# Kernel tuning notes

Measured on AMD Instinct MI355X. Metric: run time of the kernel, lower is better.

The kernel has to match this reference:

```python
import jax, jax.numpy as jnp
import numpy as np
import math

L, K, B = 16, 2048, 2
BATCH = 4
N = K * B


def _pe(k, b_beats):
    # PositionalEncoding buffer: pe[features_dim=K, num_of_beats=B]
    pos = jnp.arange(k, dtype=jnp.float32)[:, None]                      # (K, 1)
    div = jnp.exp(jnp.arange(0, b_beats, 2, dtype=jnp.float32) * (-math.log(10000.0) / b_beats))
    pe = jnp.zeros((k, b_beats), dtype=jnp.float32)
    pe = pe.at[:, 0::2].set(jnp.sin(pos * div))
    pe = pe.at[:, 1::2].set(jnp.cos(pos * div))
    return pe                                                            # (K, B)


def setup_inputs() -> dict:
    key = jax.random.key(0)
    ks = jax.random.split(key, 10)
    return {
        "X": jax.random.normal(ks[0], (BATCH, L, N), jnp.float32),
        "S": jax.random.normal(ks[1], (BATCH, L, N), jnp.float32),
        "W_1x": jax.random.normal(ks[2], (L, L), jnp.float32),
        "W_1s": jax.random.normal(ks[3], (L, L), jnp.float32),
        "W_2x": jax.random.normal(ks[4], (K, K), jnp.float32),
        "W_2s": jax.random.normal(ks[5], (K, K), jnp.float32),
        "conv_wx": jax.random.normal(ks[6], (2 * L, 2 * L, 3, 3), jnp.float32) * 0.05,
        "conv_bx": jnp.zeros((2 * L,), jnp.float32),
        "conv_ws": jax.random.normal(ks[7], (2 * L, 2 * L, 3, 3), jnp.float32) * 0.05,
        "conv_bs": jnp.zeros((2 * L,), jnp.float32),
    }


def _branch(E, W2):
    # E: (b, L, N). A = softmax(E^T E, axis=2); Ea = E @ A; then K-dim mixing by W2.
    b = E.shape[0]
    A = jax.nn.softmax(jnp.einsum('bln,blm->bnm', E, E), axis=2)         # (b, N, N)
    Ea = jnp.einsum('bln,bnm->blm', E, A)                                # (b, L, N)
    Ea4 = Ea.reshape(b, L, K, B)
    M = jnp.einsum('blkt,kj->bljt', Ea4, W2)                             # (b, L, K, B)
    return M.reshape(b, L, N)


def _conv(x, w, bias):
    y = jax.lax.conv_general_dilated(x, w, (1, 1), 'SAME',
                                     dimension_numbers=('NCHW', 'OIHW', 'NCHW'))
    return y + bias[None, :, None, None]


def reference(X, S, W_1x, W_1s, W_2x, W_2s, conv_wx, conv_bx, conv_ws, conv_bs):
    b = X.shape[0]
    Xe = jnp.einsum('bln,lm->bmn', S, W_1x)
    Se = jnp.einsum('bln,lm->bmn', X, W_1s)
    Mx = _branch(Xe, W_2x)
    Ms = _branch(Se, W_2s)
    X_hat = jnp.concatenate((Mx * X, X), axis=1).reshape(b, 2 * L, K, B)
    S_hat = jnp.concatenate((Ms * S, S), axis=1).reshape(b, 2 * L, K, B)
    # positional encoding broadcast over (batch, 2L); dropout in eval mode = identity
    S_hat = S_hat + _pe(K, B)[None, None]
    X_e_hat = _conv(X_hat, conv_wx, conv_bx)
    S_e_hat = _conv(S_hat, conv_ws, conv_bs)
    return jnp.concatenate((X_e_hat, S_e_hat), axis=1)                   # (b, 4L, K, B)
```

## Files before the change

kernel.cpp:

```cpp
#include <hip/hip_runtime.h>
#include <math.h>

#define TPB 256

static constexpr int LL = 16;
static constexpr int KK = 2048;
static constexpr int NBATCH = 4;
static constexpr int NN = 4096;
static constexpr int BBR = 8;

static constexpr size_t OFF_EHL = 0;
static constexpr size_t OFF_ET  = 524288;
static constexpr size_t OFF_EAT = 819200;
static constexpr size_t OFF_PB  = 2129920;
static constexpr size_t OFF_PMX = 3178496;
static constexpr size_t OFF_PSM = 3244032;
static constexpr size_t OFF_PMM = 3309568;

typedef unsigned short ushortT;
typedef __attribute__((ext_vector_type(8))) short short8v;
typedef __attribute__((ext_vector_type(4))) float f32x4;
typedef __attribute__((ext_vector_type(16))) float f32x16;

__device__ __forceinline__ ushortT f2bf(float x) {
  union { float f; unsigned int u; } c; c.f = x;
  unsigned int u = c.u;
  return (ushortT)((u + 0x7FFFu + ((u >> 16) & 1u)) >> 16);
}
__device__ __forceinline__ float bf2f(ushortT h) {
  union { unsigned int u; float f; } c; c.u = ((unsigned int)h) << 16;
  return c.f;
}
__device__ __forceinline__ float exp2a(float x) {
  float r; asm("v_exp_f32 %0, %1" : "=v"(r) : "v"(x)); return r;
}

__global__ __launch_bounds__(TPB) void prep_kernel(
    const float* __restrict__ X, const float* __restrict__ S,
    const float* __restrict__ W1x, const float* __restrict__ W1s,
    ushortT* __restrict__ Ehl, ushortT* __restrict__ Ept) {
  __shared__ float wsh[256];
  __shared__ ushortT tl[16][272];
  const int tid = threadIdx.x;
  const int br = blockIdx.z;
  wsh[tid] = br ? W1s[tid] : W1x[tid];
  __syncthreads();
  const int n0 = blockIdx.x * 256;
  const int b = blockIdx.y;
  const int n = n0 + tid;
  const float SC = 1.2011224087f;
  const int wq = tid & 31;
  const int slot = (wq < 16) ? ((wq >> 2) * 8 + (wq & 3))
                             : (((wq - 16) >> 2) * 8 + 4 + (wq & 3));
  const int ptid = (tid & ~31) | slot;
  const float* In = br ? X : S;

  float in[16];
#pragma unroll
  for (int l = 0; l < 16; ++l)
    in[l] = In[(size_t)(b * 16 + l) * NN + n];
  float e[16];
#pragma unroll
  for (int m = 0; m < 16; ++m) {
    float a0 = 0.f;
#pragma unroll
    for (int l = 0; l < 16; ++l) a0 = fmaf(in[l], wsh[l * 16 + m], a0);
    e[m] = a0;
  }
  const int bbr = br * 4 + b;
  unsigned int rw[16];
#pragma unroll
  for (int q = 0; q < 16; ++q) rw[q] = 0;
#pragma unroll
  for (int k = 0; k < 16; ++k) {
    const float vs = e[k] * SC;
    ushortT h = f2bf(vs);
    ushortT lo = f2bf(vs - bf2f(h));
    rw[k >> 1] |= ((unsigned int)h) << (16 * (k & 1));
    rw[8 + (k >> 1)] |= ((unsigned int)lo) << (16 * (k & 1));
    tl[k][ptid] = f2bf(e[k]);
  }
  uint4* dst = (uint4*)(Ehl + ((size_t)bbr * NN + n) * 32);
  dst[0] = make_uint4(rw[0], rw[1], rw[2], rw[3]);
  dst[1] = make_uint4(rw[4], rw[5], rw[6], rw[7]);
  dst[2] = make_uint4(rw[8], rw[9], rw[10], rw[11]);
  dst[3] = make_uint4(rw[12], rw[13], rw[14], rw[15]);
  __syncthreads();
  {
    const int r = tid >> 4, c0 = (tid & 15) * 16;
    const uint4* src = (const uint4*)(&tl[r][c0]);
    uint4* d2 = (uint4*)(Ept + ((size_t)bbr * 16 + r) * NN + n0 + c0);
    d2[0] = src[0];
    d2[1] = src[1];
  }
}

__global__ __launch_bounds__(TPB) void passA_kernel(
    const ushortT* __restrict__ Ehl, float* __restrict__ pmx,
    float* __restrict__ psm) {
  const int bid = blockIdx.x;
  const int bbr = bid & 7;
  const int ms = (bid >> 3) & 1;
  const int n0 = (bid >> 4) * 64;
  const int tid = threadIdx.x;
  const int w = tid >> 6, lane = tid & 63;
  const int lc = lane & 31;
  const int koff = (lane >> 5) * 8;
  const ushortT* Eb = Ehl + (size_t)bbr * NN * 32;

  short8v bh[2], bl[2];
#pragma unroll
  for (int s = 0; s < 2; ++s) {
    const ushortT* rp = Eb + (size_t)(n0 + s * 32 + lc) * 32;
    bh[s] = *(const short8v*)(rp + koff);
    bl[s] = *(const short8v*)(rp + 16 + koff);
  }
  float mx[2] = {-INFINITY, -INFINITY};
  float sm[2] = {0.f, 0.f};
  const f32x16 z16 = {0.f, 0.f, 0.f, 0.f, 0.f, 0.f, 0.f, 0.f,
                      0.f, 0.f, 0.f, 0.f, 0.f, 0.f, 0.f, 0.f};
  const ushortT* ap = Eb + (size_t)(ms * 2048 + w * 512 + lc) * 32;
  for (int ch = 0; ch < 16; ++ch) {
    short8v ah = *(const short8v*)(ap + koff);
    short8v al = *(const short8v*)(ap + 16 + koff);
    ap += 32 * 32;
#pragma unroll
    for (int s = 0; s < 2; ++s) {
      f32x16 c = __builtin_amdgcn_mfma_f32_32x32x16_bf16(ah, bh[s], z16, 0, 0, 0);
      c = __builtin_amdgcn_mfma_f32_32x32x16_bf16(al, bh[s], c, 0, 0, 0);
      c = __builtin_amdgcn_mfma_f32_32x32x16_bf16(ah, bl[s], c, 0, 0, 0);
      float t0 = fmaxf(fmaxf(c[0], c[1]), fmaxf(c[2], c[3]));
      float t1 = fmaxf(fmaxf(c[4], c[5]), fmaxf(c[6], c[7]));
      float t2 = fmaxf(fmaxf(c[8], c[9]), fmaxf(c[10], c[11]));
      float t3 = fmaxf(fmaxf(c[12], c[13]), fmaxf(c[14], c[15]));
      float tm = fmaxf(fmaxf(t0, t1), fmaxf(t2, t3));
      if (tm > mx[s] + 30.f) {
        sm[s] *= exp2a(mx[s] - tm);
        mx[s] = tm;
      }
      float e0 = exp2a(c[0] - mx[s]) + exp2a(c[1] - mx[s]);
      float e1 = exp2a(c[2] - mx[s]) + exp2a(c[3] - mx[s]);
      float e2 = exp2a(c[4] - mx[s]) + exp2a(c[5] - mx[s]);
      float e3 = exp2a(c[6] - mx[s]) + exp2a(c[7] - mx[s]);
      float e4 = exp2a(c[8] - mx[s]) + exp2a(c[9] - mx[s]);
      float e5 = exp2a(c[10] - mx[s]) + exp2a(c[11] - mx[s]);
      float e6 = exp2a(c[12] - mx[s]) + exp2a(c[13] - mx[s]);
      float e7 = exp2a(c[14] - mx[s]) + exp2a(c[15] - mx[s]);
      sm[s] += ((e0 + e1) + (e2 + e3)) + ((e4 + e5) + (e6 + e7));
    }
  }
#pragma unroll
  for (int s = 0; s < 2; ++s) {
    float omx = __shfl_xor(mx[s], 32);
    float osm = __shfl_xor(sm[s], 32);
    float nm = fmaxf(mx[s], omx);
    sm[s] = sm[s] * exp2a(mx[s] - nm) + osm * exp2a(omx - nm);
    mx[s] = nm;
  }
  __shared__ float smx[4][2][32], ssm[4][2][32];
  if (lane < 32) {
#pragma unroll
    for (int s = 0; s < 2; ++s) {
      smx[w][s][lc] = mx[s];
      ssm[w][s][lc] = sm[s];
    }
  }
  __syncthreads();
  if (tid < 64) {
    const int s = tid >> 5, col = tid & 31;
    float M = fmaxf(fmaxf(smx[0][s][col], smx[1][s][col]),
                    fmaxf(smx[2][s][col], smx[3][s][col]));
    float Ssum = ssm[0][s][col] * exp2a(smx[0][s][col] - M) +
                 ssm[1][s][col] * exp2a(smx[1][s][col] - M) +
                 ssm[2][s][col] * exp2a(smx[2][s][col] - M) +
                 ssm[3][s][col] * exp2a(smx[3][s][col] - M);
    const size_t o = (size_t)(ms * 8 + bbr) * NN + n0 + s * 32 + col;
    pmx[o] = M;
    psm[o] = Ssum;
  }
}

__global__ __launch_bounds__(TPB) void passB_kernel(
    const ushortT* __restrict__ Ehl, const ushortT* __restrict__ Ept,
    const float* __restrict__ pmx, const float* __restrict__ psm,
    float* __restrict__ pb) {
  const int bid = blockIdx.x;
  const int bbr = bid & 7;
  const int ns = (bid >> 3) & 1;
  const int m0 = (bid >> 4) * 64;
  const int tid = threadIdx.x;
  const int w = tid >> 6, lane = tid & 63;
  const int lr = lane & 15, g = lane >> 4;
  const ushortT* Eb = Ehl + (size_t)bbr * NN * 32;
  const ushortT* Tb = Ept + (size_t)bbr * 16 * NN;
  __shared__ float lsb[2048];
  __shared__ float red[4][4][16][17];
  for (int i = tid; i < 2048; i += TPB) {
    const size_t base = (size_t)bbr * NN + ns * 2048 + i;
    float m0v = pmx[base], m1v = pmx[32768 + base];
    float s0v = psm[base], s1v = psm[32768 + base];
    float M = fmaxf(m0v, m1v);
    float Ssum = s0v * exp2a(m0v - M) + s1v * exp2a(m1v - M);
    lsb[i] = -(M + log2f(fmaxf(Ssum, 1e-38f)));
  }
  __syncthreads();

  const short8v zero8 = {0, 0, 0, 0, 0, 0, 0, 0};
  short8v b1[4], b2[4];
#pragma unroll
  for (int s = 0; s < 4; ++s) {
    const ushortT* rp = Eb + (size_t)(m0 + s * 16 + lr) * 32;
    b1[s] = *(const short8v*)(rp + (g & 1) * 8);
    b2[s] = zero8;
    if (g < 2) b2[s] = *(const short8v*)(rp + 16 + g * 8);
  }
  f32x4 acc[4] = {{0.f, 0.f, 0.f, 0.f}, {0.f, 0.f, 0.f, 0.f},
                  {0.f, 0.f, 0.f, 0.f}, {0.f, 0.f, 0.f, 0.f}};
  const ushortT* ap = Eb + (size_t)(ns * 2048 + w * 512 + lr) * 32 + g * 8;
  const ushortT* vp = Tb + (size_t)lr * NN + ns * 2048 + w * 512 + g * 8;
  const float* lp = lsb + w * 512 + g * 4;
#pragma unroll 2
  for (int ch = 0; ch < 16; ++ch) {
    short8v a0 = *(const short8v*)ap;
    short8v a1 = *(const short8v*)(ap + 16 * 32);
    short8v ae = *(const short8v*)vp;
    f32x4 sd0 = *(const f32x4*)lp;
    f32x4 sd1 = *(const f32x4*)(lp + 16);
    ap += 32 * 32; vp += 32; lp += 32;
#pragma unroll
    for (int s = 0; s < 4; ++s) {
      f32x4 c0 = __builtin_amdgcn_mfma_f32_16x16x32_bf16(a0, b1[s], sd0, 0, 0, 0);
      c0 = __builtin_amdgcn_mfma_f32_16x16x32_bf16(a0, b2[s], c0, 0, 0, 0);
      f32x4 c1 = __builtin_amdgcn_mfma_f32_16x16x32_bf16(a1, b1[s], sd1, 0, 0, 0);
      c1 = __builtin_amdgcn_mfma_f32_16x16x32_bf16(a1, b2[s], c1, 0, 0, 0);
      float p0 = exp2a(c0[0]), p1 = exp2a(c0[1]);
      float p2 = exp2a(c0[2]), p3 = exp2a(c0[3]);
      float q0 = exp2a(c1[0]), q1 = exp2a(c1[1]);
      float q2 = exp2a(c1[2]), q3 = exp2a(c1[3]);
      unsigned int u0, u1, u2, u3;
      asm("v_cvt_pk_bf16_f32 %0, %1, %2" : "=v"(u0) : "v"(p0), "v"(p1));
      asm("v_cvt_pk_bf16_f32 %0, %1, %2" : "=v"(u1) : "v"(p2), "v"(p3));
      asm("v_cvt_pk_bf16_f32 %0, %1, %2" : "=v"(u2) : "v"(q0), "v"(q1));
      asm("v_cvt_pk_bf16_f32 %0, %1, %2" : "=v"(u3) : "v"(q2), "v"(q3));
      const uint4 uv = make_uint4(u0, u1, u2, u3);
      const short8v pf = __builtin_bit_cast(short8v, uv);
      acc[s] = __builtin_amdgcn_mfma_f32_16x16x32_bf16(ae, pf, acc[s], 0, 0, 0);
    }
  }
#pragma unroll
  for (int s = 0; s < 4; ++s)
#pragma unroll
    for (int r = 0; r < 4; ++r) red[w][s][g * 4 + r][lr] = acc[s][r];
  __syncthreads();
  for (int o = tid; o < 1024; o += TPB) {
    const int s = o >> 8, l = (o >> 4) & 15, mm = o & 15;
    float v = red[0][s][l][mm] + red[1][s][l][mm] +
              red[2][s][l][mm] + red[3][s][l][mm];
    pb[((size_t)(ns * 8 + bbr) * 16 + l) * NN + m0 + s * 16 + mm] = v;
  }
}

__global__ __launch_bounds__(TPB) void reduceB_kernel(
    const float* __restrict__ pb, ushortT* __restrict__ EaT) {
  const int gidx = blockIdx.x * TPB + threadIdx.x;
  const int r = gidx >> 10;
  const int j4 = gidx & 1023;
  const float4 p0 = *(const float4*)(pb + (size_t)r * NN + j4 * 4);
  const float4 p1 = *(const float4*)(pb + (size_t)(128 + r) * NN + j4 * 4);
  const float v0 = p0.x + p1.x, v1 = p0.y + p1.y;
  const float v2 = p0.z + p1.z, v3 = p0.w + p1.w;
  const int bbr = r >> 4, l = r & 15;
  unsigned int ue, uo;
  asm("v_cvt_pk_bf16_f32 %0, %1, %2" : "=v"(ue) : "v"(v0), "v"(v2));
  asm("v_cvt_pk_bf16_f32 %0, %1, %2" : "=v"(uo) : "v"(v1), "v"(v3));
  *(unsigned int*)(EaT + ((size_t)(bbr * 2 + 0) * 16 + l) * KK + j4 * 2) = ue;
  *(unsigned int*)(EaT + ((size_t)(bbr * 2 + 1) * 16 + l) * KK + j4 * 2) = uo;
}

__global__ __launch_bounds__(TPB) void mmix_kernel(
    const ushortT* __restrict__ EaT,
    const float* __restrict__ W2x, const float* __restrict__ W2s,
    float* __restrict__ pmm) {
  const int jt = blockIdx.x;
  const int br = blockIdx.y;
  const int ks = blockIdx.z;
  const float* W2 = br ? W2s : W2x;
  const int j0 = jt * 16;
  const int kb = ks * 512;
  const int tid = threadIdx.x;
  const int w = tid >> 6, lane = tid & 63;
  const int b = w;
  const int lj = tid & 15, kp0 = tid >> 4;
  const int fl = lane & 15, g = lane >> 4;
  __shared__ ushortT bpan[2][16][72];

  const size_t rb0 = ((size_t)(br * 4 + b) * 2 + 0) * 16;
  const size_t rb1 = ((size_t)(br * 4 + b) * 2 + 1) * 16;

  f32x4 acc0 = {0.f, 0.f, 0.f, 0.f};
  f32x4 acc1 = {0.f, 0.f, 0.f, 0.f};

  float r0, r1, r2, r3;
  r0 = W2[(size_t)(kb + 2 * kp0)      * KK + j0 + lj];
  r1 = W2[(size_t)(kb + 2 * kp0 + 1)  * KK + j0 + lj];
  r2 = W2[(size_t)(kb + 2 * kp0 + 32) * KK + j0 + lj];
  r3 = W2[(size_t)(kb + 2 * kp0 + 33) * KK + j0 + lj];

  for (int c = 0; c < 8; ++c) {
    const int cur = c & 1;
    unsigned int u0, u1;
    asm("v_cvt_pk_bf16_f32 %0, %1, %2" : "=v"(u0) : "v"(r0), "v"(r1));
    asm("v_cvt_pk_bf16_f32 %0, %1, %2" : "=v"(u1) : "v"(r2), "v"(r3));
    *(unsigned int*)(&bpan[cur][lj][kp0 * 2]) = u0;
    *(unsigned int*)(&bpan[cur][lj][(kp0 + 16) * 2]) = u1;
    __syncthreads();
    if (c < 7) {
      const int kc = kb + (c + 1) * 64;
      r0 = W2[(size_t)(kc + 2 * kp0)      * KK + j0 + lj];
      r1 = W2[(size_t)(kc + 2 * kp0 + 1)  * KK + j0 + lj];
      r2 = W2[(size_t)(kc + 2 * kp0 + 32) * KK + j0 + lj];
      r3 = W2[(size_t)(kc + 2 * kp0 + 33) * KK + j0 + lj];
    }
#pragma unroll
    for (int s = 0; s < 2; ++s) {
      const int k = kb + c * 64 + s * 32 + g * 8;
      short8v bf = *(const short8v*)(&bpan[cur][fl][s * 32 + g * 8]);
      short8v a0 = *(const short8v*)(EaT + (rb0 + fl) * (size_t)KK + k);
      short8v a1 = *(const short8v*)(EaT + (rb1 + fl) * (size_t)KK + k);
      acc0 = __builtin_amdgcn_mfma_f32_16x16x32_bf16(a0, bf, acc0, 0, 0, 0);
      acc1 = __builtin_amdgcn_mfma_f32_16x16x32_bf16(a1, bf, acc1, 0, 0, 0);
    }
    __syncthreads();
  }

  const int j = j0 + fl;
#pragma unroll
  for (int r = 0; r < 4; ++r) {
    const int l = g * 4 + r;
    const size_t base = ((size_t)(ks * 2 + br) * 4 + b) * 2;
    pmm[((base + 0) * 16 + l) * (size_t)KK + j] = acc0[r];
    pmm[((base + 1) * 16 + l) * (size_t)KK + j] = acc1[r];
  }
}

__global__ __launch_bounds__(TPB) void conv_kernel(
    const float* __restrict__ pmm,
    const float* __restrict__ X, const float* __restrict__ S,
    const float* __restrict__ Wx, const float* __restrict__ Bx,
    const float* __restrict__ Ws, const float* __restrict__ Bs,
    float* __restrict__ out) {
  const int kt = blockIdx.x;
  const int b = blockIdx.y;
  const int br = blockIdx.z;
  const float* Wt = br ? Ws : Wx;
  const float* Bi = br ? Bs : Bx;
  const float* Inp = br ? S : X;
  __shared__ float inT[32 * 34 * 2];
  __shared__ float wts[32 * 289];
  const int tid = threadIdx.x;
  const int k0 = kt * 32;

  for (int f = tid; f < 32 * 288; f += TPB) {
    const int c = f / 288, rem = f % 288;
    wts[c * 289 + rem] = Wt[f];
  }
  for (int f = tid; f < 32 * 34 * 2; f += TPB) {
    const int ch = f / 68, rem = f % 68;
    const int kk = rem >> 1, t = rem & 1;
    const int j = k0 - 1 + kk;
    float v = 0.f;
    if (j >= 0 && j < KK) {
      const int l = ch & 15;
      const float inv = Inp[(size_t)(b * 16 + l) * NN + 2 * j + t];
      if (ch < 16) {
        float sum = 0.f;
#pragma unroll
        for (int ks = 0; ks < 4; ++ks)
          sum += pmm[((((size_t)(ks * 2 + br) * 4 + b) * 2 + t) * 16 + l) *
                         (size_t)KK + j];
        if (br == 0) {
          v = sum * inv;
        } else {
          const float pe = t ? cosf((float)j) : sinf((float)j);
          v = fmaf(sum, inv, pe);
        }
      } else {
        if (br == 0) {
          v = inv;
        } else {
          const float pe = t ? cosf((float)j) : sinf((float)j);
          v = inv + pe;
        }
      }
    }
    inT[f] = v;
  }
  __syncthreads();

  const int c = tid >> 3, sub = tid & 7;
  const float bias = Bi[c];
  float acc0[4], acc1[4];
#pragma unroll
  for (int i = 0; i < 4; ++i) { acc0[i] = bias; acc1[i] = bias; }

  for (int cin = 0; cin < 32; ++cin) {
    const float* wp = wts + c * 289 + cin * 9;
    const float w00 = wp[0], w01 = wp[1], w02 = wp[2];
    const float w10 = wp[3], w11 = wp[4], w12 = wp[5];
    const float w20 = wp[6], w21 = wp[7], w22 = wp[8];
    const float* ip = inT + cin * 68;
#pragma unroll
    for (int i = 0; i < 4; ++i) {
      const int kl = sub + 8 * i;
      const float* q = ip + kl * 2;
      const float i00 = q[0], i01 = q[1];
      const float i10 = q[2], i11 = q[3];
      const float i20 = q[4], i21 = q[5];
      acc0[i] = fmaf(i00, w01, acc0[i]); acc0[i] = fmaf(i01, w02, acc0[i]);
      acc0[i] = fmaf(i10, w11, acc0[i]); acc0[i] = fmaf(i11, w12, acc0[i]);
      acc0[i] = fmaf(i20, w21, acc0[i]); acc0[i] = fmaf(i21, w22, acc0[i]);
      acc1[i] = fmaf(i00, w00, acc1[i]); acc1[i] = fmaf(i01, w01, acc1[i]);
      acc1[i] = fmaf(i10, w10, acc1[i]); acc1[i] = fmaf(i11, w11, acc1[i]);
      acc1[i] = fmaf(i20, w20, acc1[i]); acc1[i] = fmaf(i21, w21, acc1[i]);
    }
  }
#pragma unroll
  for (int i = 0; i < 4; ++i) {
    const int k = k0 + sub + 8 * i;
    const size_t o = ((size_t)(b * 64 + br * 32 + c) * KK + k) * 2;
    out[o] = acc0[i];
    out[o + 1] = acc1[i];
  }
}

extern "C" void kernel_launch(void* const* d_in, const int* in_sizes, int n_in,
                              void* d_out, int out_size, void* d_ws, size_t ws_size,
                              hipStream_t stream) {
  (void)in_sizes; (void)n_in; (void)out_size; (void)ws_size;
  const float* X   = (const float*)d_in[0];
  const float* S   = (const float*)d_in[1];
  const float* W1x = (const float*)d_in[2];
  const float* W1s = (const float*)d_in[3];
  const float* W2x = (const float*)d_in[4];
  const float* W2s = (const float*)d_in[5];
  const float* Cwx = (const float*)d_in[6];
  const float* Cbx = (const float*)d_in[7];
  const float* Cws = (const float*)d_in[8];
  const float* Cbs = (const float*)d_in[9];
  float* out = (float*)d_out;
  float* ws = (float*)d_ws;

  ushortT* Ehl = (ushortT*)(ws + OFF_EHL);
  ushortT* Ept = (ushortT*)(ws + OFF_ET);
  ushortT* EaT = (ushortT*)(ws + OFF_EAT);
  float*   pb  = ws + OFF_PB;
  float*   pmx = ws + OFF_PMX;
  float*   psm = ws + OFF_PSM;
  float*   pmm = ws + OFF_PMM;

  hipLaunchKernelGGL(prep_kernel, dim3(16, NBATCH, 2), dim3(TPB), 0, stream,
                     X, S, W1x, W1s, Ehl, Ept);
  hipLaunchKernelGGL(passA_kernel, dim3(1024), dim3(TPB), 0, stream,
                     Ehl, pmx, psm);
  hipLaunchKernelGGL(passB_kernel, dim3(1024), dim3(TPB), 0, stream,
                     Ehl, Ept, pmx, psm, pb);
  hipLaunchKernelGGL(reduceB_kernel, dim3(512), dim3(TPB), 0, stream,
                     pb, EaT);
  hipLaunchKernelGGL(mmix_kernel, dim3(128, 2, 4), dim3(TPB), 0, stream,
                     EaT, W2x, W2s, pmm);
  hipLaunchKernelGGL(conv_kernel, dim3(64, NBATCH, 2), dim3(TPB), 0, stream,
                     pmm, X, S, Cwx, Cbx, Cws, Cbs, out);
}
```

Baseline: 108.3 us.

## Remove split-N in passB and fold reduceB into passB epilogue

passB no longer splits the softmax-weighted accumulation over N into two halves. Each block now covers the full N range (32 chunks per wave instead of 16), and the grid shrinks from 1024 to 512 blocks. The partial-sum buffer and the separate reduceB kernel go away. The epilogue writes the bf16 de-interleaved EaT directly, which saves one launch plus a global write and read of partials, at the cost of half as many blocks (less parallelism) and a larger LDS lsb array.

```diff
diff --git a/kernel.cpp b/kernel.cpp
--- a/kernel.cpp
+++ b/kernel.cpp
@@ -12,7 +12,6 @@
 static constexpr size_t OFF_EHL = 0;
 static constexpr size_t OFF_ET  = 524288;
 static constexpr size_t OFF_EAT = 819200;
-static constexpr size_t OFF_PB  = 2129920;
 static constexpr size_t OFF_PMX = 3178496;
 static constexpr size_t OFF_PSM = 3244032;
 static constexpr size_t OFF_PMM = 3309568;
@@ -183,20 +182,19 @@
 __global__ __launch_bounds__(TPB) void passB_kernel(
     const ushortT* __restrict__ Ehl, const ushortT* __restrict__ Ept,
     const float* __restrict__ pmx, const float* __restrict__ psm,
-    float* __restrict__ pb) {
+    ushortT* __restrict__ EaT) {
   const int bid = blockIdx.x;
   const int bbr = bid & 7;
-  const int ns = (bid >> 3) & 1;
-  const int m0 = (bid >> 4) * 64;
+  const int m0 = (bid >> 3) * 64;
   const int tid = threadIdx.x;
   const int w = tid >> 6, lane = tid & 63;
   const int lr = lane & 15, g = lane >> 4;
   const ushortT* Eb = Ehl + (size_t)bbr * NN * 32;
   const ushortT* Tb = Ept + (size_t)bbr * 16 * NN;
-  __shared__ float lsb[2048];
+  __shared__ float lsb[4096];
   __shared__ float red[4][4][16][17];
-  for (int i = tid; i < 2048; i += TPB) {
-    const size_t base = (size_t)bbr * NN + ns * 2048 + i;
+  for (int i = tid; i < 4096; i += TPB) {
+    const size_t base = (size_t)bbr * NN + i;
     float m0v = pmx[base], m1v = pmx[32768 + base];
     float s0v = psm[base], s1v = psm[32768 + base];
     float M = fmaxf(m0v, m1v);
@@ -216,11 +214,11 @@
   }
   f32x4 acc[4] = {{0.f, 0.f, 0.f, 0.f}, {0.f, 0.f, 0.f, 0.f},
                   {0.f, 0.f, 0.f, 0.f}, {0.f, 0.f, 0.f, 0.f}};
-  const ushortT* ap = Eb + (size_t)(ns * 2048 + w * 512 + lr) * 32 + g * 8;
-  const ushortT* vp = Tb + (size_t)lr * NN + ns * 2048 + w * 512 + g * 8;
-  const float* lp = lsb + w * 512 + g * 4;
+  const ushortT* ap = Eb + (size_t)(w * 1024 + lr) * 32 + g * 8;
+  const ushortT* vp = Tb + (size_t)lr * NN + w * 1024 + g * 8;
+  const float* lp = lsb + w * 1024 + g * 4;
 #pragma unroll 2
-  for (int ch = 0; ch < 16; ++ch) {
+  for (int ch = 0; ch < 32; ++ch) {
     short8v a0 = *(const short8v*)ap;
     short8v a1 = *(const short8v*)(ap + 16 * 32);
     short8v ae = *(const short8v*)vp;
@@ -256,25 +254,9 @@
     const int s = o >> 8, l = (o >> 4) & 15, mm = o & 15;
     float v = red[0][s][l][mm] + red[1][s][l][mm] +
               red[2][s][l][mm] + red[3][s][l][mm];
-    pb[((size_t)(ns * 8 + bbr) * 16 + l) * NN + m0 + s * 16 + mm] = v;
-  }
-}
-
-__global__ __launch_bounds__(TPB) void reduceB_kernel(
-    const float* __restrict__ pb, ushortT* __restrict__ EaT) {
-  const int gidx = blockIdx.x * TPB + threadIdx.x;
-  const int r = gidx >> 10;
-  const int j4 = gidx & 1023;
-  const float4 p0 = *(const float4*)(pb + (size_t)r * NN + j4 * 4);
-  const float4 p1 = *(const float4*)(pb + (size_t)(128 + r) * NN + j4 * 4);
-  const float v0 = p0.x + p1.x, v1 = p0.y + p1.y;
-  const float v2 = p0.z + p1.z, v3 = p0.w + p1.w;
-  const int bbr = r >> 4, l = r & 15;
-  unsigned int ue, uo;
-  asm("v_cvt_pk_bf16_f32 %0, %1, %2" : "=v"(ue) : "v"(v0), "v"(v2));
-  asm("v_cvt_pk_bf16_f32 %0, %1, %2" : "=v"(uo) : "v"(v1), "v"(v3));
-  *(unsigned int*)(EaT + ((size_t)(bbr * 2 + 0) * 16 + l) * KK + j4 * 2) = ue;
-  *(unsigned int*)(EaT + ((size_t)(bbr * 2 + 1) * 16 + l) * KK + j4 * 2) = uo;
+    const int M = m0 + s * 16 + mm;
+    EaT[((size_t)(bbr * 2 + (M & 1)) * 16 + l) * (size_t)KK + (M >> 1)] = f2bf(v);
+  }
 }
 
 __global__ __launch_bounds__(TPB) void mmix_kernel(
@@ -365,14 +347,14 @@
     wts[c * 289 + rem] = Wt[f];
   }
   for (int f = tid; f < 32 * 34 * 2; f += TPB) {
-    const int ch = f / 68, rem = f % 68;
+    const int cin = f / 68, rem = f % 68;
     const int kk = rem >> 1, t = rem & 1;
     const int j = k0 - 1 + kk;
     float v = 0.f;
     if (j >= 0 && j < KK) {
-      const int l = ch & 15;
+      const int l = cin & 15;
       const float inv = Inp[(size_t)(b * 16 + l) * NN + 2 * j + t];
-      if (ch < 16) {
+      if (cin < 16) {
         float sum = 0.f;
 #pragma unroll
         for (int ks = 0; ks < 4; ++ks)
@@ -453,7 +435,6 @@
   ushortT* Ehl = (ushortT*)(ws + OFF_EHL);
   ushortT* Ept = (ushortT*)(ws + OFF_ET);
   ushortT* EaT = (ushortT*)(ws + OFF_EAT);
-  float*   pb  = ws + OFF_PB;
   float*   pmx = ws + OFF_PMX;
   float*   psm = ws + OFF_PSM;
   float*   pmm = ws + OFF_PMM;
@@ -462,10 +443,8 @@
                      X, S, W1x, W1s, Ehl, Ept);
   hipLaunchKernelGGL(passA_kernel, dim3(1024), dim3(TPB), 0, stream,
                      Ehl, pmx, psm);
-  hipLaunchKernelGGL(passB_kernel, dim3(1024), dim3(TPB), 0, stream,
-                     Ehl, Ept, pmx, psm, pb);
-  hipLaunchKernelGGL(reduceB_kernel, dim3(512), dim3(TPB), 0, stream,
-                     pb, EaT);
+  hipLaunchKernelGGL(passB_kernel, dim3(512), dim3(TPB), 0, stream,
+                     Ehl, Ept, pmx, psm, EaT);
   hipLaunchKernelGGL(mmix_kernel, dim3(128, 2, 4), dim3(TPB), 0, stream,
                      EaT, W2x, W2s, pmm);
   hipLaunchKernelGGL(conv_kernel, dim3(64, NBATCH, 2), dim3(TPB), 0, stream,
```

Result: slower. 110.5 us (+2.0%).
